# Optimization experiments

Measured on AMD Instinct MI355X. Metric: run time of the kernel, lower is better.

The kernel has to match this reference:

```python
import jax, jax.numpy as jnp
import numpy as np

B, N, D, H, DK, DV = 2, 2048, 1024, 16, 64, 64
NEG = -1000000000.0
EPS = 1e-6


def setup_inputs() -> dict:
    key = jax.random.key(0)
    ks = jax.random.split(key, 8)
    s = 0.02
    return {
        "q": jax.random.normal(ks[0], (B, N, D), jnp.float32),
        "k": jax.random.normal(ks[1], (B, N, D), jnp.float32),
        "v": jax.random.normal(ks[2], (B, N, D), jnp.float32),
        "attn_mask": jnp.ones((B, N, N), jnp.int32),
        "Wq": jax.random.normal(ks[3], (D, H * DK), jnp.float32) * s,
        "Wk": jax.random.normal(ks[4], (D, H * DK), jnp.float32) * s,
        "Wv": jax.random.normal(ks[5], (D, H * DV), jnp.float32) * s,
        "Wo": jax.random.normal(ks[6], (H * DV, D), jnp.float32) * s,
        "gamma": jnp.ones((D,), jnp.float32),
        "beta": jnp.zeros((D,), jnp.float32),
    }


def reference(q, k, v, attn_mask, Wq, Wk, Wv, Wo, gamma, beta):
    b, n, _ = q.shape
    residual = q
    # project and split heads: (b, h, n, dk)
    qh = (q @ Wq).reshape(b, n, H, DK).transpose(0, 2, 1, 3)
    kh = (k @ Wk).reshape(b, n, H, DK).transpose(0, 2, 1, 3)
    vh = (v @ Wv).reshape(b, n, H, DV).transpose(0, 2, 1, 3)
    temperature = DK ** 0.5
    scores = jnp.einsum('bhnd,bhmd->bhnm', qh / temperature, kh)
    # external mask (masked where mask == 0), broadcast over heads
    scores = jnp.where(attn_mask[:, None, :, :] == 0, NEG, scores)
    # built-in causal mask (strictly upper triangle)
    causal = jnp.triu(jnp.ones((n, n), dtype=bool), k=1)
    scores = jnp.where(causal, NEG, scores)
    attn = jax.nn.softmax(scores, axis=-1)
    out = jnp.einsum('bhnm,bhmd->bnhd', attn, vh).reshape(b, n, H * DV)
    out = out @ Wo + residual
    # LayerNorm(eps=1e-6)
    mean = out.mean(-1, keepdims=True)
    var = ((out - mean) ** 2).mean(-1, keepdims=True)
    out = (out - mean) / jnp.sqrt(var + EPS) * gamma + beta
    return out, attn
```

## Files before the change

### kernel.cpp

```cpp
#include <hip/hip_runtime.h>
#include <hip/hip_bf16.h>
#include <stdint.h>

#define B_ 2
#define N_ 2048
#define D_ 1024
#define H_ 16
#define MM 4096
#define NN 1024
#define KK 1024

typedef __bf16 bf16;
typedef __bf16 bf16x8 __attribute__((ext_vector_type(8)));
typedef float f32x4 __attribute__((ext_vector_type(4)));

struct __align__(8) bf4 { bf16 v[4]; };

#define LDS_STRIDE 144
#define LOG2E 1.44269504088896340736f

#define GLDS(gp, lp)                                                     \
    __builtin_amdgcn_global_load_lds(                                    \
        (const __attribute__((address_space(1))) void*)(gp),             \
        (__attribute__((address_space(3))) void*)(lp), 16, 0, 0)

__global__ __launch_bounds__(256) void k_cvt3(const float* __restrict__ q,
                                              const float* __restrict__ k,
                                              const float* __restrict__ v,
                                              bf16* __restrict__ qb,
                                              bf16* __restrict__ kb,
                                              bf16* __restrict__ vb) {
    const int z = blockIdx.y;
    const float* s = z == 0 ? q : z == 1 ? k : v;
    bf16* d = z == 0 ? qb : z == 1 ? kb : vb;
    size_t i = ((size_t)blockIdx.x * 256 + threadIdx.x) * 8;
    f32x4 a = *(const f32x4*)(s + i);
    f32x4 b = *(const f32x4*)(s + i + 4);
    bf16x8 o;
#pragma unroll
    for (int j = 0; j < 4; ++j) { o[j] = (bf16)a[j]; o[4 + j] = (bf16)b[j]; }
    *(bf16x8*)(d + i) = o;
}

__global__ void k_wtt4(const float* __restrict__ Wq, const float* __restrict__ Wk,
                       const float* __restrict__ Wv, const float* __restrict__ Wo,
                       bf16* __restrict__ WqT, bf16* __restrict__ WkT,
                       bf16* __restrict__ WvT, bf16* __restrict__ WoT) {
    const int z = blockIdx.z;
    const float* W = z == 0 ? Wq : z == 1 ? Wk : z == 2 ? Wv : Wo;
    bf16* Wt = z == 0 ? WqT : z == 1 ? WkT : z == 2 ? WvT : WoT;
    __shared__ float t[32][33];
    int bx = blockIdx.x * 32, by = blockIdx.y * 32;
    int tx = threadIdx.x, ty = threadIdx.y;
#pragma unroll
    for (int j = 0; j < 32; j += 8)
        t[ty + j][tx] = W[(size_t)(by + ty + j) * 1024 + bx + tx];
    __syncthreads();
#pragma unroll
    for (int j = 0; j < 32; j += 8)
        Wt[(size_t)(bx + ty + j) * 1024 + by + tx] = (bf16)t[tx][ty + j];
}

__global__ __launch_bounds__(256) void k_bits(const int* __restrict__ mask,
                                              uint32_t* __restrict__ bits) {
    size_t flat = (size_t)blockIdx.x * 256 + threadIdx.x;
    int col = (int)(flat & (N_ - 1));
    int row = (int)((flat >> 11) & (N_ - 1));
    bool ok = (mask[flat] != 0) && (col <= row);
    unsigned long long bal = __ballot(ok);
    if ((threadIdx.x & 63) == 0)
        *(unsigned long long*)(bits + (flat >> 5)) = bal;
}

__device__ __forceinline__ void mm_core(const bf16* __restrict__ A,
                                        const bf16* __restrict__ Bt,
                                        int bm0, int bn0,
                                        bf16* As, bf16* Bs,
                                        f32x4 (&acc)[4][4]) {
    const int tid = threadIdx.x, w = tid >> 6, lane = tid & 63;
    const int g = lane >> 4, li = lane & 15;
    const int wr = w >> 1, wc = w & 1;

    f32x4 zz = {0.f, 0.f, 0.f, 0.f};
#pragma unroll
    for (int mf = 0; mf < 4; ++mf)
#pragma unroll
        for (int nf = 0; nf < 4; ++nf) acc[mf][nf] = zz;

    auto stage = [&](int k0) {
#pragma unroll
        for (int c = 0; c < 4; ++c) {
            int ch = c * 256 + tid;
            int r = ch >> 3, cl = ch & 7;
            GLDS(A + (size_t)(bm0 + r) * KK + k0 + cl * 8,
                 As + ((size_t)c * 256 + w * 64) * 8);
        }
#pragma unroll
        for (int c = 0; c < 4; ++c) {
            int ch = c * 256 + tid;
            int r = ch >> 3, cl = ch & 7;
            GLDS(Bt + (size_t)(bn0 + r) * KK + k0 + cl * 8,
                 Bs + ((size_t)c * 256 + w * 64) * 8);
        }
    };

    stage(0);
    for (int s = 0; s < KK / 64; ++s) {
        __syncthreads();
#pragma unroll
        for (int kk = 0; kk < 2; ++kk) {
            bf16x8 af[4], bfr[4];
#pragma unroll
            for (int i = 0; i < 4; ++i) {
                af[i] = *(const bf16x8*)(As + (wr * 64 + i * 16 + li) * 64 + kk * 32 + g * 8);
                bfr[i] = *(const bf16x8*)(Bs + (wc * 64 + i * 16 + li) * 64 + kk * 32 + g * 8);
            }
#pragma unroll
            for (int mf = 0; mf < 4; ++mf)
#pragma unroll
                for (int nf = 0; nf < 4; ++nf)
                    acc[mf][nf] = __builtin_amdgcn_mfma_f32_16x16x32_bf16(
                        af[mf], bfr[nf], acc[mf][nf], 0, 0, 0);
        }
        __syncthreads();
        if (s + 1 < KK / 64) stage((s + 1) * 64);
    }
}

__global__ __launch_bounds__(256) void k_proj(const bf16* __restrict__ qb,
                                              const bf16* __restrict__ kb,
                                              const bf16* __restrict__ vb,
                                              const bf16* __restrict__ WqT,
                                              const bf16* __restrict__ WkT,
                                              const bf16* __restrict__ WvT,
                                              bf16* __restrict__ Qh,
                                              bf16* __restrict__ Kh,
                                              bf16* __restrict__ Vt) {
    __shared__ __align__(16) bf16 As[128 * 64];
    __shared__ __align__(16) bf16 Bs[128 * 64];
    const int z = blockIdx.y;
    const bf16* A = z == 0 ? qb : z == 1 ? kb : vb;
    const bf16* Bt = z == 0 ? WqT : z == 1 ? WkT : WvT;
    int bid = blockIdx.x;
    int swz = (bid & 7) * 32 + (bid >> 3);
    int bm0 = (swz >> 3) * 128, bn0 = (swz & 7) * 128;

    f32x4 acc[4][4];
    mm_core(A, Bt, bm0, bn0, As, Bs, acc);

    const int tid = threadIdx.x, w = tid >> 6, lane = tid & 63;
    const int g = lane >> 4, li = lane & 15;
    const int wr = w >> 1, wc = w & 1;
    const float scale = (z == 0) ? 0.125f * LOG2E : 1.0f;

    if (z < 2) {
        bf16* C = (z == 0) ? Qh : Kh;
#pragma unroll
        for (int mf = 0; mf < 4; ++mf)
#pragma unroll
            for (int nf = 0; nf < 4; ++nf) {
                int m0 = bm0 + wr * 64 + mf * 16 + g * 4;
                int n = bn0 + wc * 64 + nf * 16 + li;
#pragma unroll
                for (int r = 0; r < 4; ++r)
                    C[(size_t)(m0 + r) * NN + n] = (bf16)(acc[mf][nf][r] * scale);
            }
    } else {
#pragma unroll
        for (int mf = 0; mf < 4; ++mf)
#pragma unroll
            for (int nf = 0; nf < 4; ++nf) {
                int m0 = bm0 + wr * 64 + mf * 16 + g * 4;
                int n = bn0 + wc * 64 + nf * 16 + li;
                int bq = m0 >> 11, tok = m0 & (N_ - 1);
                int hh = n >> 6, dv = n & 63;
                bf4 val;
#pragma unroll
                for (int r = 0; r < 4; ++r) val.v[r] = (bf16)acc[mf][nf][r];
                *(bf4*)(Vt + ((size_t)((bq * H_ + hh) * 64 + dv)) * N_ + tok) = val;
            }
    }
}

__global__ __launch_bounds__(256) void k_out(const bf16* __restrict__ Ob,
                                             const bf16* __restrict__ WoT,
                                             float* __restrict__ outp,
                                             const float* __restrict__ resid) {
    __shared__ __align__(16) bf16 As[128 * 64];
    __shared__ __align__(16) bf16 Bs[128 * 64];
    int bid = blockIdx.x;
    int swz = (bid & 7) * 32 + (bid >> 3);
    int bm0 = (swz >> 3) * 128, bn0 = (swz & 7) * 128;

    f32x4 acc[4][4];
    mm_core(Ob, WoT, bm0, bn0, As, Bs, acc);

    const int tid = threadIdx.x, w = tid >> 6, lane = tid & 63;
    const int g = lane >> 4, li = lane & 15;
    const int wr = w >> 1, wc = w & 1;
#pragma unroll
    for (int mf = 0; mf < 4; ++mf)
#pragma unroll
        for (int nf = 0; nf < 4; ++nf) {
            int m0 = bm0 + wr * 64 + mf * 16 + g * 4;
            int n = bn0 + wc * 64 + nf * 16 + li;
#pragma unroll
            for (int r = 0; r < 4; ++r) {
                size_t ix = (size_t)(m0 + r) * NN + n;
                outp[ix] = acc[mf][nf][r] + resid[ix];
            }
        }
}

__global__ __launch_bounds__(256) void k_attn(const bf16* __restrict__ Qh,
                                              const bf16* __restrict__ Kh,
                                              const bf16* __restrict__ Vt,
                                              const uint32_t* __restrict__ bits,
                                              float* __restrict__ attnp,
                                              bf16* __restrict__ Ob) {
    __shared__ __align__(16) char Qs[64 * LDS_STRIDE];
    __shared__ __align__(16) char Ks[64 * LDS_STRIDE];
    __shared__ __align__(16) char Vs[64 * LDS_STRIDE];
    __shared__ __align__(16) char Ps[64 * LDS_STRIDE];
    const int tid = threadIdx.x, lane = tid & 63, w = tid >> 6;
    const int g = lane >> 4, li = lane & 15;
    const int p = blockIdx.x, h = blockIdx.y, b = blockIdx.z;
    const int srow = tid >> 3, sc = tid & 7;
    const int myrow = w * 16 + li;

    const size_t kbase = ((size_t)b * N_) * D_ + h * 64;
    const size_t vbase = ((size_t)(b * H_ + h) * 64) * N_;
    f32x4 zz = {0.f, 0.f, 0.f, 0.f};

    for (int half = 0; half < 2; ++half) {
        const int qt = half ? (31 - p) : p;
        const int i0 = qt << 6;
        const size_t abase = (((size_t)b * H_ + h) * N_ + i0) * (size_t)N_;

        __syncthreads();
        {
            const char* qsrc = (const char*)Qh +
                (kbase + (size_t)(i0 + srow) * D_ + sc * 8) * 2;
            bf16x8 t0 = *(const bf16x8*)qsrc;
            bf16x8 t1 = *(const bf16x8*)(qsrc + (size_t)32 * D_ * 2);
            *(bf16x8*)(Qs + srow * LDS_STRIDE + sc * 16) = t0;
            *(bf16x8*)(Qs + (srow + 32) * LDS_STRIDE + sc * 16) = t1;
        }
        const uint32_t* mrow = bits + (((size_t)b * N_ + i0 + myrow) << 6);

        float m = -1e30f, l = 0.f;
        bf16x8 ka, kb2, va, vb2;
        {
            const char* ks = (const char*)Kh + (kbase + (size_t)srow * D_ + sc * 8) * 2;
            ka = *(const bf16x8*)ks;
            kb2 = *(const bf16x8*)(ks + (size_t)32 * D_ * 2);
        }
        for (int jt = 0; jt <= qt; ++jt) {
            __syncthreads();
            *(bf16x8*)(Ks + srow * LDS_STRIDE + sc * 16) = ka;
            *(bf16x8*)(Ks + (srow + 32) * LDS_STRIDE + sc * 16) = kb2;
            {
                int jn = (jt < qt) ? jt + 1 : qt;
                const char* ks = (const char*)Kh +
                    (kbase + (size_t)(jn * 64 + srow) * D_ + sc * 8) * 2;
                ka = *(const bf16x8*)ks;
                kb2 = *(const bf16x8*)(ks + (size_t)32 * D_ * 2);
            }
            uint2 mw = *(const uint2*)(mrow + (jt << 1));
            __syncthreads();

            f32x4 s[4];
#pragma unroll
            for (int mf = 0; mf < 4; ++mf) s[mf] = zz;
#pragma unroll
            for (int kk = 0; kk < 2; ++kk) {
                const int kb = kk * 64 + (g << 4);
                bf16x8 qf = *(const bf16x8*)(Qs + myrow * LDS_STRIDE + kb);
#pragma unroll
                for (int mf = 0; mf < 4; ++mf) {
                    bf16x8 kf = *(const bf16x8*)(Ks + (mf * 16 + li) * LDS_STRIDE + kb);
                    s[mf] = __builtin_amdgcn_mfma_f32_16x16x32_bf16(kf, qf, s[mf], 0, 0, 0);
                }
            }
            float tmax = m;
#pragma unroll
            for (int mf = 0; mf < 4; ++mf) {
                uint32_t wsel = (mf < 2) ? mw.x : mw.y;
#pragma unroll
                for (int r = 0; r < 4; ++r) {
                    int sh = (mf & 1) * 16 + g * 4 + r;
                    float xv = ((wsel >> sh) & 1) ? s[mf][r] : -1e9f;
                    s[mf][r] = xv;
                    tmax = fmaxf(tmax, xv);
                }
            }
            tmax = fmaxf(tmax, __shfl_xor(tmax, 16));
            tmax = fmaxf(tmax, __shfl_xor(tmax, 32));
            float ps = 0.f;
#pragma unroll
            for (int mf = 0; mf < 4; ++mf)
#pragma unroll
                for (int r = 0; r < 4; ++r) ps += exp2f(s[mf][r] - tmax);
            ps += __shfl_xor(ps, 16);
            ps += __shfl_xor(ps, 32);
            l = l * exp2f(m - tmax) + ps;
            m = tmax;
        }
        const float ml = m + __log2f(l);

        f32x4 oacc[4];
#pragma unroll
        for (int nf = 0; nf < 4; ++nf) oacc[nf] = zz;

        {
            const char* ks = (const char*)Kh + (kbase + (size_t)srow * D_ + sc * 8) * 2;
            ka = *(const bf16x8*)ks;
            kb2 = *(const bf16x8*)(ks + (size_t)32 * D_ * 2);
            const char* vs = (const char*)Vt + (vbase + (size_t)srow * N_ + sc * 8) * 2;
            va = *(const bf16x8*)vs;
            vb2 = *(const bf16x8*)(vs + (size_t)32 * N_ * 2);
        }
        for (int jt = 0; jt <= qt; ++jt) {
            __syncthreads();
            *(bf16x8*)(Ks + srow * LDS_STRIDE + sc * 16) = ka;
            *(bf16x8*)(Ks + (srow + 32) * LDS_STRIDE + sc * 16) = kb2;
            *(bf16x8*)(Vs + srow * LDS_STRIDE + sc * 16) = va;
            *(bf16x8*)(Vs + (srow + 32) * LDS_STRIDE + sc * 16) = vb2;
            {
                int jn = (jt < qt) ? jt + 1 : qt;
                const char* ks = (const char*)Kh +
                    (kbase + (size_t)(jn * 64 + srow) * D_ + sc * 8) * 2;
                ka = *(const bf16x8*)ks;
                kb2 = *(const bf16x8*)(ks + (size_t)32 * D_ * 2);
                const char* vs = (const char*)Vt +
                    (vbase + (size_t)srow * N_ + jn * 64 + sc * 8) * 2;
                va = *(const bf16x8*)vs;
                vb2 = *(const bf16x8*)(vs + (size_t)32 * N_ * 2);
            }
            uint2 mw = *(const uint2*)(mrow + (jt << 1));
            __syncthreads();

            f32x4 s[4];
#pragma unroll
            for (int mf = 0; mf < 4; ++mf) s[mf] = zz;
#pragma unroll
            for (int kk = 0; kk < 2; ++kk) {
                const int kb = kk * 64 + (g << 4);
                bf16x8 qf = *(const bf16x8*)(Qs + myrow * LDS_STRIDE + kb);
#pragma unroll
                for (int mf = 0; mf < 4; ++mf) {
                    bf16x8 kf = *(const bf16x8*)(Ks + (mf * 16 + li) * LDS_STRIDE + kb);
                    s[mf] = __builtin_amdgcn_mfma_f32_16x16x32_bf16(kf, qf, s[mf], 0, 0, 0);
                }
            }

#pragma unroll
            for (int mf = 0; mf < 4; ++mf) {
                uint32_t wsel = (mf < 2) ? mw.x : mw.y;
#pragma unroll
                for (int r = 0; r < 4; ++r) {
                    int sh = (mf & 1) * 16 + g * 4 + r;
                    float xv = ((wsel >> sh) & 1) ? s[mf][r] : -1e9f;
                    s[mf][r] = exp2f(xv - ml);
                }
                __builtin_nontemporal_store(s[mf],
                    (f32x4*)(attnp + abase + (size_t)myrow * N_ + (jt << 6) + mf * 16 + g * 4));
                bf4 pk;
#pragma unroll
                for (int r = 0; r < 4; ++r) pk.v[r] = (bf16)s[mf][r];
                *(bf4*)(Ps + myrow * LDS_STRIDE + (mf * 16 + g * 4) * 2) = pk;
            }
#pragma unroll
            for (int kk = 0; kk < 2; ++kk) {
                const int kb = kk * 64 + (g << 4);
                bf16x8 pf = *(const bf16x8*)(Ps + myrow * LDS_STRIDE + kb);
#pragma unroll
                for (int nf = 0; nf < 4; ++nf) {
                    bf16x8 vf = *(const bf16x8*)(Vs + (nf * 16 + li) * LDS_STRIDE + kb);
                    oacc[nf] = __builtin_amdgcn_mfma_f32_16x16x32_bf16(pf, vf, oacc[nf], 0, 0, 0);
                }
            }
        }
#pragma unroll
        for (int nf = 0; nf < 4; ++nf)
#pragma unroll
            for (int r = 0; r < 4; ++r) {
                int gi = i0 + w * 16 + g * 4 + r;
                Ob[((size_t)(b * N_ + gi)) * D_ + h * 64 + nf * 16 + li] = (bf16)oacc[nf][r];
            }
        int zc0 = i0 + 64;
        if (zc0 < N_) {
            int r = tid >> 2, tc = tid & 3;
            f32x4 z = zz;
            for (int c = zc0 + tc * 4; c < N_; c += 16)
                __builtin_nontemporal_store(z, (f32x4*)(attnp + abase + (size_t)r * N_ + c));
        }
    }
}

__global__ __launch_bounds__(256) void k_ln(float* __restrict__ out,
                                            const float* __restrict__ gamma,
                                            const float* __restrict__ beta) {
    const int row = blockIdx.x, t = threadIdx.x, lane = t & 63, w = t >> 6;
    float* p = out + (size_t)row * D_;
    f32x4 x = *(const f32x4*)(p + t * 4);
    float s = x[0] + x[1] + x[2] + x[3];
    float s2 = x[0] * x[0] + x[1] * x[1] + x[2] * x[2] + x[3] * x[3];
#pragma unroll
    for (int o = 1; o < 64; o <<= 1) {
        s += __shfl_xor(s, o);
        s2 += __shfl_xor(s2, o);
    }
    __shared__ float r1[4], r2[4];
    if (lane == 0) { r1[w] = s; r2[w] = s2; }
    __syncthreads();
    s = r1[0] + r1[1] + r1[2] + r1[3];
    s2 = r2[0] + r2[1] + r2[2] + r2[3];
    float mean = s * (1.f / D_);
    float var = s2 * (1.f / D_) - mean * mean;
    float rstd = rsqrtf(var + 1e-6f);
    f32x4 gv = *(const f32x4*)(gamma + t * 4);
    f32x4 bv = *(const f32x4*)(beta + t * 4);
    f32x4 y;
#pragma unroll
    for (int c = 0; c < 4; ++c) y[c] = (x[c] - mean) * rstd * gv[c] + bv[c];
    *(f32x4*)(p + t * 4) = y;
}

extern "C" void kernel_launch(void* const* d_in, const int* in_sizes, int n_in,
                              void* d_out, int out_size, void* d_ws,
                              size_t ws_size, hipStream_t stream) {
    (void)in_sizes; (void)n_in; (void)out_size; (void)ws_size;
    const float* q = (const float*)d_in[0];
    const float* k = (const float*)d_in[1];
    const float* v = (const float*)d_in[2];
    const int* msk = (const int*)d_in[3];
    const float* Wq = (const float*)d_in[4];
    const float* Wk = (const float*)d_in[5];
    const float* Wv = (const float*)d_in[6];
    const float* Wo = (const float*)d_in[7];
    const float* gamma = (const float*)d_in[8];
    const float* beta = (const float*)d_in[9];

    float* outp = (float*)d_out;
    float* attnp = outp + (size_t)B_ * N_ * D_;

    const size_t U = (size_t)B_ * N_ * D_;
    const size_t W1 = (size_t)D_ * D_;
    bf16* ws = (bf16*)d_ws;
    bf16* qb = ws;   ws += U;
    bf16* kb = ws;   ws += U;
    bf16* vb = ws;   ws += U;
    bf16* WqT = ws;  ws += W1;
    bf16* WkT = ws;  ws += W1;
    bf16* WvT = ws;  ws += W1;
    bf16* WoT = ws;  ws += W1;
    bf16* Qh = ws;   ws += U;
    bf16* Kh = ws;   ws += U;
    bf16* Vt = ws;   ws += U;
    bf16* Ob = ws;   ws += U;
    uint32_t* bits = (uint32_t*)ws;

    k_cvt3<<<dim3(U / 8 / 256, 3), 256, 0, stream>>>(q, k, v, qb, kb, vb);
    k_wtt4<<<dim3(32, 32, 4), dim3(32, 8), 0, stream>>>(Wq, Wk, Wv, Wo, WqT, WkT, WvT, WoT);
    k_bits<<<(size_t)B_ * N_ * N_ / 256, 256, 0, stream>>>(msk, bits);

    k_proj<<<dim3(256, 3), 256, 0, stream>>>(qb, kb, vb, WqT, WkT, WvT, Qh, Kh, Vt);

    k_attn<<<dim3(16, H_, B_), 256, 0, stream>>>(Qh, Kh, Vt, bits, attnp, Ob);

    k_out<<<256, 256, 0, stream>>>(Ob, WoT, outp, q);

    k_ln<<<B_ * N_, 256, 0, stream>>>(outp, gamma, beta);
}
```

Baseline: 306.8 us.

## Fuse fp32-to-bf16 input conversion into projection GEMM and flatten attention grid

Drops the separate q/k/v conversion kernel: the projection GEMM now loads fp32 activations into registers, converts them to bf16 and writes them to a padded LDS tile, with the next tile's global loads overlapping the current tile's MFMA work. This removes one full read/write pass of the activations and a launch, at the cost of register-staged loads instead of direct global-to-LDS copies. The attention kernel changes from blocks that each process a paired query tile (p and 31-p) sequentially to a 1024-block grid with one query tile per block, ordered so short and long tiles interleave. Its attention-matrix stores also switch from nontemporal to ordinary stores.

```diff
diff --git a/kernel.cpp b/kernel.cpp
--- a/kernel.cpp
+++ b/kernel.cpp
@@ -23,24 +23,6 @@
     __builtin_amdgcn_global_load_lds(                                    \
         (const __attribute__((address_space(1))) void*)(gp),             \
         (__attribute__((address_space(3))) void*)(lp), 16, 0, 0)
-
-__global__ __launch_bounds__(256) void k_cvt3(const float* __restrict__ q,
-                                              const float* __restrict__ k,
-                                              const float* __restrict__ v,
-                                              bf16* __restrict__ qb,
-                                              bf16* __restrict__ kb,
-                                              bf16* __restrict__ vb) {
-    const int z = blockIdx.y;
-    const float* s = z == 0 ? q : z == 1 ? k : v;
-    bf16* d = z == 0 ? qb : z == 1 ? kb : vb;
-    size_t i = ((size_t)blockIdx.x * 256 + threadIdx.x) * 8;
-    f32x4 a = *(const f32x4*)(s + i);
-    f32x4 b = *(const f32x4*)(s + i + 4);
-    bf16x8 o;
-#pragma unroll
-    for (int j = 0; j < 4; ++j) { o[j] = (bf16)a[j]; o[4 + j] = (bf16)b[j]; }
-    *(bf16x8*)(d + i) = o;
-}
 
 __global__ void k_wtt4(const float* __restrict__ Wq, const float* __restrict__ Wk,
                        const float* __restrict__ Wv, const float* __restrict__ Wo,
@@ -72,87 +54,95 @@
         *(unsigned long long*)(bits + (flat >> 5)) = bal;
 }
 
-__device__ __forceinline__ void mm_core(const bf16* __restrict__ A,
-                                        const bf16* __restrict__ Bt,
-                                        int bm0, int bn0,
-                                        bf16* As, bf16* Bs,
-                                        f32x4 (&acc)[4][4]) {
-    const int tid = threadIdx.x, w = tid >> 6, lane = tid & 63;
-    const int g = lane >> 4, li = lane & 15;
-    const int wr = w >> 1, wc = w & 1;
-
-    f32x4 zz = {0.f, 0.f, 0.f, 0.f};
-#pragma unroll
-    for (int mf = 0; mf < 4; ++mf)
-#pragma unroll
-        for (int nf = 0; nf < 4; ++nf) acc[mf][nf] = zz;
-
-    auto stage = [&](int k0) {
-#pragma unroll
-        for (int c = 0; c < 4; ++c) {
-            int ch = c * 256 + tid;
-            int r = ch >> 3, cl = ch & 7;
-            GLDS(A + (size_t)(bm0 + r) * KK + k0 + cl * 8,
-                 As + ((size_t)c * 256 + w * 64) * 8);
-        }
-#pragma unroll
-        for (int c = 0; c < 4; ++c) {
-            int ch = c * 256 + tid;
-            int r = ch >> 3, cl = ch & 7;
-            GLDS(Bt + (size_t)(bn0 + r) * KK + k0 + cl * 8,
-                 Bs + ((size_t)c * 256 + w * 64) * 8);
-        }
-    };
-
-    stage(0);
-    for (int s = 0; s < KK / 64; ++s) {
-        __syncthreads();
-#pragma unroll
-        for (int kk = 0; kk < 2; ++kk) {
-            bf16x8 af[4], bfr[4];
-#pragma unroll
-            for (int i = 0; i < 4; ++i) {
-                af[i] = *(const bf16x8*)(As + (wr * 64 + i * 16 + li) * 64 + kk * 32 + g * 8);
-                bfr[i] = *(const bf16x8*)(Bs + (wc * 64 + i * 16 + li) * 64 + kk * 32 + g * 8);
-            }
-#pragma unroll
-            for (int mf = 0; mf < 4; ++mf)
-#pragma unroll
-                for (int nf = 0; nf < 4; ++nf)
-                    acc[mf][nf] = __builtin_amdgcn_mfma_f32_16x16x32_bf16(
-                        af[mf], bfr[nf], acc[mf][nf], 0, 0, 0);
-        }
-        __syncthreads();
-        if (s + 1 < KK / 64) stage((s + 1) * 64);
-    }
-}
-
-__global__ __launch_bounds__(256) void k_proj(const bf16* __restrict__ qb,
-                                              const bf16* __restrict__ kb,
-                                              const bf16* __restrict__ vb,
+__global__ __launch_bounds__(256) void k_proj(const float* __restrict__ qf,
+                                              const float* __restrict__ kf,
+                                              const float* __restrict__ vf,
                                               const bf16* __restrict__ WqT,
                                               const bf16* __restrict__ WkT,
                                               const bf16* __restrict__ WvT,
                                               bf16* __restrict__ Qh,
                                               bf16* __restrict__ Kh,
                                               bf16* __restrict__ Vt) {
-    __shared__ __align__(16) bf16 As[128 * 64];
+    __shared__ __align__(16) bf16 As[128 * 72];
     __shared__ __align__(16) bf16 Bs[128 * 64];
     const int z = blockIdx.y;
-    const bf16* A = z == 0 ? qb : z == 1 ? kb : vb;
+    const float* A = z == 0 ? qf : z == 1 ? kf : vf;
     const bf16* Bt = z == 0 ? WqT : z == 1 ? WkT : WvT;
     int bid = blockIdx.x;
     int swz = (bid & 7) * 32 + (bid >> 3);
     int bm0 = (swz >> 3) * 128, bn0 = (swz & 7) * 128;
 
-    f32x4 acc[4][4];
-    mm_core(A, Bt, bm0, bn0, As, Bs, acc);
-
     const int tid = threadIdx.x, w = tid >> 6, lane = tid & 63;
     const int g = lane >> 4, li = lane & 15;
     const int wr = w >> 1, wc = w & 1;
+
+    f32x4 zz = {0.f, 0.f, 0.f, 0.f};
+    f32x4 acc[4][4];
+#pragma unroll
+    for (int mf = 0; mf < 4; ++mf)
+#pragma unroll
+        for (int nf = 0; nf < 4; ++nf) acc[mf][nf] = zz;
+
+    f32x4 pa[4][2];
+    auto issueA = [&](int k0) {
+#pragma unroll
+        for (int c = 0; c < 4; ++c) {
+            int ch = c * 256 + tid;
+            int r = ch >> 3, cl = ch & 7;
+            const float* s = A + (size_t)(bm0 + r) * KK + k0 + cl * 8;
+            pa[c][0] = *(const f32x4*)s;
+            pa[c][1] = *(const f32x4*)(s + 4);
+        }
+    };
+    auto writeA = [&]() {
+#pragma unroll
+        for (int c = 0; c < 4; ++c) {
+            int ch = c * 256 + tid;
+            int r = ch >> 3, cl = ch & 7;
+            bf16x8 t;
+#pragma unroll
+            for (int j = 0; j < 4; ++j) {
+                t[j] = (bf16)pa[c][0][j];
+                t[4 + j] = (bf16)pa[c][1][j];
+            }
+            *(bf16x8*)(As + (size_t)r * 72 + cl * 8) = t;
+        }
+    };
+    auto stageB = [&](int k0) {
+#pragma unroll
+        for (int c = 0; c < 4; ++c) {
+            int ch = c * 256 + tid;
+            int r = ch >> 3, cl = ch & 7;
+            GLDS(Bt + (size_t)(bn0 + r) * KK + k0 + cl * 8,
+                 Bs + ((size_t)c * 256 + w * 64) * 8);
+        }
+    };
+
+    issueA(0);
+    for (int s = 0; s < KK / 64; ++s) {
+        __syncthreads();
+        writeA();
+        stageB(s * 64);
+        if (s + 1 < KK / 64) issueA((s + 1) * 64);
+        __syncthreads();
+#pragma unroll
+        for (int kk = 0; kk < 2; ++kk) {
+            bf16x8 af[4], bfr[4];
+#pragma unroll
+            for (int i = 0; i < 4; ++i) {
+                af[i] = *(const bf16x8*)(As + (wr * 64 + i * 16 + li) * 72 + kk * 32 + g * 8);
+                bfr[i] = *(const bf16x8*)(Bs + (wc * 64 + i * 16 + li) * 64 + kk * 32 + g * 8);
+            }
+#pragma unroll
+            for (int mf = 0; mf < 4; ++mf)
+#pragma unroll
+                for (int nf = 0; nf < 4; ++nf)
+                    acc[mf][nf] = __builtin_amdgcn_mfma_f32_16x16x32_bf16(
+                        af[mf], bfr[nf], acc[mf][nf], 0, 0, 0);
+        }
+    }
+
     const float scale = (z == 0) ? 0.125f * LOG2E : 1.0f;
-
     if (z < 2) {
         bf16* C = (z == 0) ? Qh : Kh;
 #pragma unroll
@@ -192,12 +182,55 @@
     int swz = (bid & 7) * 32 + (bid >> 3);
     int bm0 = (swz >> 3) * 128, bn0 = (swz & 7) * 128;
 
-    f32x4 acc[4][4];
-    mm_core(Ob, WoT, bm0, bn0, As, Bs, acc);
-
     const int tid = threadIdx.x, w = tid >> 6, lane = tid & 63;
     const int g = lane >> 4, li = lane & 15;
     const int wr = w >> 1, wc = w & 1;
+
+    f32x4 zz = {0.f, 0.f, 0.f, 0.f};
+    f32x4 acc[4][4];
+#pragma unroll
+    for (int mf = 0; mf < 4; ++mf)
+#pragma unroll
+        for (int nf = 0; nf < 4; ++nf) acc[mf][nf] = zz;
+
+    auto stage = [&](int k0) {
+#pragma unroll
+        for (int c = 0; c < 4; ++c) {
+            int ch = c * 256 + tid;
+            int r = ch >> 3, cl = ch & 7;
+            GLDS(Ob + (size_t)(bm0 + r) * KK + k0 + cl * 8,
+                 As + ((size_t)c * 256 + w * 64) * 8);
+        }
+#pragma unroll
+        for (int c = 0; c < 4; ++c) {
+            int ch = c * 256 + tid;
+            int r = ch >> 3, cl = ch & 7;
+            GLDS(WoT + (size_t)(bn0 + r) * KK + k0 + cl * 8,
+                 Bs + ((size_t)c * 256 + w * 64) * 8);
+        }
+    };
+
+    stage(0);
+    for (int s = 0; s < KK / 64; ++s) {
+        __syncthreads();
+#pragma unroll
+        for (int kk = 0; kk < 2; ++kk) {
+            bf16x8 af[4], bfr[4];
+#pragma unroll
+            for (int i = 0; i < 4; ++i) {
+                af[i] = *(const bf16x8*)(As + (wr * 64 + i * 16 + li) * 64 + kk * 32 + g * 8);
+                bfr[i] = *(const bf16x8*)(Bs + (wc * 64 + i * 16 + li) * 64 + kk * 32 + g * 8);
+            }
+#pragma unroll
+            for (int mf = 0; mf < 4; ++mf)
+#pragma unroll
+                for (int nf = 0; nf < 4; ++nf)
+                    acc[mf][nf] = __builtin_amdgcn_mfma_f32_16x16x32_bf16(
+                        af[mf], bfr[nf], acc[mf][nf], 0, 0, 0);
+        }
+        __syncthreads();
+        if (s + 1 < KK / 64) stage((s + 1) * 64);
+    }
 #pragma unroll
     for (int mf = 0; mf < 4; ++mf)
 #pragma unroll
@@ -224,177 +257,177 @@
     __shared__ __align__(16) char Ps[64 * LDS_STRIDE];
     const int tid = threadIdx.x, lane = tid & 63, w = tid >> 6;
     const int g = lane >> 4, li = lane & 15;
-    const int p = blockIdx.x, h = blockIdx.y, b = blockIdx.z;
     const int srow = tid >> 3, sc = tid & 7;
     const int myrow = w * 16 + li;
 
+    const int id = blockIdx.x;
+    const int s_ = id & 255, g_ = id >> 8;
+    const int u = s_ & 31;
+    const int hb = (s_ >> 5) | (g_ << 3);
+    const int h = hb & 15, b = hb >> 4;
+    const int qt = (g_ & 1) ? (31 - u) : u;
+    const int i0 = qt << 6;
+
     const size_t kbase = ((size_t)b * N_) * D_ + h * 64;
     const size_t vbase = ((size_t)(b * H_ + h) * 64) * N_;
+    const size_t abase = (((size_t)b * H_ + h) * N_ + i0) * (size_t)N_;
     f32x4 zz = {0.f, 0.f, 0.f, 0.f};
 
-    for (int half = 0; half < 2; ++half) {
-        const int qt = half ? (31 - p) : p;
-        const int i0 = qt << 6;
-        const size_t abase = (((size_t)b * H_ + h) * N_ + i0) * (size_t)N_;
-
-        __syncthreads();
+    {
+        const char* qsrc = (const char*)Qh +
+            (kbase + (size_t)(i0 + srow) * D_ + sc * 8) * 2;
+        bf16x8 t0 = *(const bf16x8*)qsrc;
+        bf16x8 t1 = *(const bf16x8*)(qsrc + (size_t)32 * D_ * 2);
+        *(bf16x8*)(Qs + srow * LDS_STRIDE + sc * 16) = t0;
+        *(bf16x8*)(Qs + (srow + 32) * LDS_STRIDE + sc * 16) = t1;
+    }
+    const uint32_t* mrow = bits + (((size_t)b * N_ + i0 + myrow) << 6);
+
+    float m = -1e30f, l = 0.f;
+    bf16x8 ka, kb2, va, vb2;
+    {
+        const char* ks = (const char*)Kh + (kbase + (size_t)srow * D_ + sc * 8) * 2;
+        ka = *(const bf16x8*)ks;
+        kb2 = *(const bf16x8*)(ks + (size_t)32 * D_ * 2);
+    }
+    for (int jt = 0; jt <= qt; ++jt) {
+        __syncthreads();
+        *(bf16x8*)(Ks + srow * LDS_STRIDE + sc * 16) = ka;
+        *(bf16x8*)(Ks + (srow + 32) * LDS_STRIDE + sc * 16) = kb2;
         {
-            const char* qsrc = (const char*)Qh +
-                (kbase + (size_t)(i0 + srow) * D_ + sc * 8) * 2;
-            bf16x8 t0 = *(const bf16x8*)qsrc;
-            bf16x8 t1 = *(const bf16x8*)(qsrc + (size_t)32 * D_ * 2);
-            *(bf16x8*)(Qs + srow * LDS_STRIDE + sc * 16) = t0;
-            *(bf16x8*)(Qs + (srow + 32) * LDS_STRIDE + sc * 16) = t1;
-        }
-        const uint32_t* mrow = bits + (((size_t)b * N_ + i0 + myrow) << 6);
-
-        float m = -1e30f, l = 0.f;
-        bf16x8 ka, kb2, va, vb2;
-        {
-            const char* ks = (const char*)Kh + (kbase + (size_t)srow * D_ + sc * 8) * 2;
+            int jn = (jt < qt) ? jt + 1 : qt;
+            const char* ks = (const char*)Kh +
+                (kbase + (size_t)(jn * 64 + srow) * D_ + sc * 8) * 2;
             ka = *(const bf16x8*)ks;
             kb2 = *(const bf16x8*)(ks + (size_t)32 * D_ * 2);
         }
-        for (int jt = 0; jt <= qt; ++jt) {
-            __syncthreads();
-            *(bf16x8*)(Ks + srow * LDS_STRIDE + sc * 16) = ka;
-            *(bf16x8*)(Ks + (srow + 32) * LDS_STRIDE + sc * 16) = kb2;
-            {
-                int jn = (jt < qt) ? jt + 1 : qt;
-                const char* ks = (const char*)Kh +
-                    (kbase + (size_t)(jn * 64 + srow) * D_ + sc * 8) * 2;
-                ka = *(const bf16x8*)ks;
-                kb2 = *(const bf16x8*)(ks + (size_t)32 * D_ * 2);
-            }
-            uint2 mw = *(const uint2*)(mrow + (jt << 1));
-            __syncthreads();
-
-            f32x4 s[4];
-#pragma unroll
-            for (int mf = 0; mf < 4; ++mf) s[mf] = zz;
-#pragma unroll
-            for (int kk = 0; kk < 2; ++kk) {
-                const int kb = kk * 64 + (g << 4);
-                bf16x8 qf = *(const bf16x8*)(Qs + myrow * LDS_STRIDE + kb);
-#pragma unroll
-                for (int mf = 0; mf < 4; ++mf) {
-                    bf16x8 kf = *(const bf16x8*)(Ks + (mf * 16 + li) * LDS_STRIDE + kb);
-                    s[mf] = __builtin_amdgcn_mfma_f32_16x16x32_bf16(kf, qf, s[mf], 0, 0, 0);
-                }
-            }
-            float tmax = m;
+        uint2 mw = *(const uint2*)(mrow + (jt << 1));
+        __syncthreads();
+
+        f32x4 s[4];
+#pragma unroll
+        for (int mf = 0; mf < 4; ++mf) s[mf] = zz;
+#pragma unroll
+        for (int kk = 0; kk < 2; ++kk) {
+            const int kb = kk * 64 + (g << 4);
+            bf16x8 qf = *(const bf16x8*)(Qs + myrow * LDS_STRIDE + kb);
 #pragma unroll
             for (int mf = 0; mf < 4; ++mf) {
-                uint32_t wsel = (mf < 2) ? mw.x : mw.y;
-#pragma unroll
-                for (int r = 0; r < 4; ++r) {
-                    int sh = (mf & 1) * 16 + g * 4 + r;
-                    float xv = ((wsel >> sh) & 1) ? s[mf][r] : -1e9f;
-                    s[mf][r] = xv;
-                    tmax = fmaxf(tmax, xv);
-                }
-            }
-            tmax = fmaxf(tmax, __shfl_xor(tmax, 16));
-            tmax = fmaxf(tmax, __shfl_xor(tmax, 32));
-            float ps = 0.f;
-#pragma unroll
-            for (int mf = 0; mf < 4; ++mf)
-#pragma unroll
-                for (int r = 0; r < 4; ++r) ps += exp2f(s[mf][r] - tmax);
-            ps += __shfl_xor(ps, 16);
-            ps += __shfl_xor(ps, 32);
-            l = l * exp2f(m - tmax) + ps;
-            m = tmax;
-        }
-        const float ml = m + __log2f(l);
-
-        f32x4 oacc[4];
-#pragma unroll
-        for (int nf = 0; nf < 4; ++nf) oacc[nf] = zz;
-
+                bf16x8 kf = *(const bf16x8*)(Ks + (mf * 16 + li) * LDS_STRIDE + kb);
+                s[mf] = __builtin_amdgcn_mfma_f32_16x16x32_bf16(kf, qf, s[mf], 0, 0, 0);
+            }
+        }
+        float tmax = m;
+#pragma unroll
+        for (int mf = 0; mf < 4; ++mf) {
+            uint32_t wsel = (mf < 2) ? mw.x : mw.y;
+#pragma unroll
+            for (int r = 0; r < 4; ++r) {
+                int sh = (mf & 1) * 16 + g * 4 + r;
+                float xv = ((wsel >> sh) & 1) ? s[mf][r] : -1e9f;
+                s[mf][r] = xv;
+                tmax = fmaxf(tmax, xv);
+            }
+        }
+        tmax = fmaxf(tmax, __shfl_xor(tmax, 16));
+        tmax = fmaxf(tmax, __shfl_xor(tmax, 32));
+        float ps = 0.f;
+#pragma unroll
+        for (int mf = 0; mf < 4; ++mf)
+#pragma unroll
+            for (int r = 0; r < 4; ++r) ps += exp2f(s[mf][r] - tmax);
+        ps += __shfl_xor(ps, 16);
+        ps += __shfl_xor(ps, 32);
+        l = l * exp2f(m - tmax) + ps;
+        m = tmax;
+    }
+    const float ml = m + __log2f(l);
+
+    f32x4 oacc[4];
+#pragma unroll
+    for (int nf = 0; nf < 4; ++nf) oacc[nf] = zz;
+
+    {
+        const char* ks = (const char*)Kh + (kbase + (size_t)srow * D_ + sc * 8) * 2;
+        ka = *(const bf16x8*)ks;
+        kb2 = *(const bf16x8*)(ks + (size_t)32 * D_ * 2);
+        const char* vs = (const char*)Vt + (vbase + (size_t)srow * N_ + sc * 8) * 2;
+        va = *(const bf16x8*)vs;
+        vb2 = *(const bf16x8*)(vs + (size_t)32 * N_ * 2);
+    }
+    for (int jt = 0; jt <= qt; ++jt) {
+        __syncthreads();
+        *(bf16x8*)(Ks + srow * LDS_STRIDE + sc * 16) = ka;
+        *(bf16x8*)(Ks + (srow + 32) * LDS_STRIDE + sc * 16) = kb2;
+        *(bf16x8*)(Vs + srow * LDS_STRIDE + sc * 16) = va;
+        *(bf16x8*)(Vs + (srow + 32) * LDS_STRIDE + sc * 16) = vb2;
         {
-            const char* ks = (const char*)Kh + (kbase + (size_t)srow * D_ + sc * 8) * 2;
+            int jn = (jt < qt) ? jt + 1 : qt;
+            const char* ks = (const char*)Kh +
+                (kbase + (size_t)(jn * 64 + srow) * D_ + sc * 8) * 2;
             ka = *(const bf16x8*)ks;
             kb2 = *(const bf16x8*)(ks + (size_t)32 * D_ * 2);
-            const char* vs = (const char*)Vt + (vbase + (size_t)srow * N_ + sc * 8) * 2;
+            const char* vs = (const char*)Vt +
+                (vbase + (size_t)srow * N_ + jn * 64 + sc * 8) * 2;
             va = *(const bf16x8*)vs;
             vb2 = *(const bf16x8*)(vs + (size_t)32 * N_ * 2);
         }
-        for (int jt = 0; jt <= qt; ++jt) {
-            __syncthreads();
-            *(bf16x8*)(Ks + srow * LDS_STRIDE + sc * 16) = ka;
-            *(bf16x8*)(Ks + (srow + 32) * LDS_STRIDE + sc * 16) = kb2;
-            *(bf16x8*)(Vs + srow * LDS_STRIDE + sc * 16) = va;
-            *(bf16x8*)(Vs + (srow + 32) * LDS_STRIDE + sc * 16) = vb2;
-            {
-                int jn = (jt < qt) ? jt + 1 : qt;
-                const char* ks = (const char*)Kh +
-                    (kbase + (size_t)(jn * 64 + srow) * D_ + sc * 8) * 2;
-                ka = *(const bf16x8*)ks;
-                kb2 = *(const bf16x8*)(ks + (size_t)32 * D_ * 2);
-                const char* vs = (const char*)Vt +
-                    (vbase + (size_t)srow * N_ + jn * 64 + sc * 8) * 2;
-                va = *(const bf16x8*)vs;
-                vb2 = *(const bf16x8*)(vs + (size_t)32 * N_ * 2);
-            }
-            uint2 mw = *(const uint2*)(mrow + (jt << 1));
-            __syncthreads();
-
-            f32x4 s[4];
-#pragma unroll
-            for (int mf = 0; mf < 4; ++mf) s[mf] = zz;
-#pragma unroll
-            for (int kk = 0; kk < 2; ++kk) {
-                const int kb = kk * 64 + (g << 4);
-                bf16x8 qf = *(const bf16x8*)(Qs + myrow * LDS_STRIDE + kb);
-#pragma unroll
-                for (int mf = 0; mf < 4; ++mf) {
-                    bf16x8 kf = *(const bf16x8*)(Ks + (mf * 16 + li) * LDS_STRIDE + kb);
-                    s[mf] = __builtin_amdgcn_mfma_f32_16x16x32_bf16(kf, qf, s[mf], 0, 0, 0);
-                }
-            }
-
+        uint2 mw = *(const uint2*)(mrow + (jt << 1));
+        __syncthreads();
+
+        f32x4 s[4];
+#pragma unroll
+        for (int mf = 0; mf < 4; ++mf) s[mf] = zz;
+#pragma unroll
+        for (int kk = 0; kk < 2; ++kk) {
+            const int kb = kk * 64 + (g << 4);
+            bf16x8 qf = *(const bf16x8*)(Qs + myrow * LDS_STRIDE + kb);
 #pragma unroll
             for (int mf = 0; mf < 4; ++mf) {
-                uint32_t wsel = (mf < 2) ? mw.x : mw.y;
-#pragma unroll
-                for (int r = 0; r < 4; ++r) {
-                    int sh = (mf & 1) * 16 + g * 4 + r;
-                    float xv = ((wsel >> sh) & 1) ? s[mf][r] : -1e9f;
-                    s[mf][r] = exp2f(xv - ml);
-                }
-                __builtin_nontemporal_store(s[mf],
-                    (f32x4*)(attnp + abase + (size_t)myrow * N_ + (jt << 6) + mf * 16 + g * 4));
-                bf4 pk;
-#pragma unroll
-                for (int r = 0; r < 4; ++r) pk.v[r] = (bf16)s[mf][r];
-                *(bf4*)(Ps + myrow * LDS_STRIDE + (mf * 16 + g * 4) * 2) = pk;
-            }
-#pragma unroll
-            for (int kk = 0; kk < 2; ++kk) {
-                const int kb = kk * 64 + (g << 4);
-                bf16x8 pf = *(const bf16x8*)(Ps + myrow * LDS_STRIDE + kb);
-#pragma unroll
-                for (int nf = 0; nf < 4; ++nf) {
-                    bf16x8 vf = *(const bf16x8*)(Vs + (nf * 16 + li) * LDS_STRIDE + kb);
-                    oacc[nf] = __builtin_amdgcn_mfma_f32_16x16x32_bf16(pf, vf, oacc[nf], 0, 0, 0);
-                }
-            }
-        }
-#pragma unroll
-        for (int nf = 0; nf < 4; ++nf)
+                bf16x8 kf = *(const bf16x8*)(Ks + (mf * 16 + li) * LDS_STRIDE + kb);
+                s[mf] = __builtin_amdgcn_mfma_f32_16x16x32_bf16(kf, qf, s[mf], 0, 0, 0);
+            }
+        }
+
+#pragma unroll
+        for (int mf = 0; mf < 4; ++mf) {
+            uint32_t wsel = (mf < 2) ? mw.x : mw.y;
 #pragma unroll
             for (int r = 0; r < 4; ++r) {
-                int gi = i0 + w * 16 + g * 4 + r;
-                Ob[((size_t)(b * N_ + gi)) * D_ + h * 64 + nf * 16 + li] = (bf16)oacc[nf][r];
-            }
-        int zc0 = i0 + 64;
-        if (zc0 < N_) {
-            int r = tid >> 2, tc = tid & 3;
-            f32x4 z = zz;
-            for (int c = zc0 + tc * 4; c < N_; c += 16)
-                __builtin_nontemporal_store(z, (f32x4*)(attnp + abase + (size_t)r * N_ + c));
-        }
+                int sh = (mf & 1) * 16 + g * 4 + r;
+                float xv = ((wsel >> sh) & 1) ? s[mf][r] : -1e9f;
+                s[mf][r] = exp2f(xv - ml);
+            }
+            *(f32x4*)(attnp + abase + (size_t)myrow * N_ + (jt << 6) + mf * 16 + g * 4) = s[mf];
+            bf4 pk;
+#pragma unroll
+            for (int r = 0; r < 4; ++r) pk.v[r] = (bf16)s[mf][r];
+            *(bf4*)(Ps + myrow * LDS_STRIDE + (mf * 16 + g * 4) * 2) = pk;
+        }
+#pragma unroll
+        for (int kk = 0; kk < 2; ++kk) {
+            const int kb = kk * 64 + (g << 4);
+            bf16x8 pf = *(const bf16x8*)(Ps + myrow * LDS_STRIDE + kb);
+#pragma unroll
+            for (int nf = 0; nf < 4; ++nf) {
+                bf16x8 vf = *(const bf16x8*)(Vs + (nf * 16 + li) * LDS_STRIDE + kb);
+                oacc[nf] = __builtin_amdgcn_mfma_f32_16x16x32_bf16(pf, vf, oacc[nf], 0, 0, 0);
+            }
+        }
+    }
+#pragma unroll
+    for (int nf = 0; nf < 4; ++nf)
+#pragma unroll
+        for (int r = 0; r < 4; ++r) {
+            int gi = i0 + w * 16 + g * 4 + r;
+            Ob[((size_t)(b * N_ + gi)) * D_ + h * 64 + nf * 16 + li] = (bf16)oacc[nf][r];
+        }
+    int zc0 = i0 + 64;
+    if (zc0 < N_) {
+        int r = tid >> 2, tc = tid & 3;
+        f32x4 z = zz;
+        for (int c = zc0 + tc * 4; c < N_; c += 16)
+            *(f32x4*)(attnp + abase + (size_t)r * N_ + c) = z;
     }
 }
 
@@ -448,9 +481,6 @@
     const size_t U = (size_t)B_ * N_ * D_;
     const size_t W1 = (size_t)D_ * D_;
     bf16* ws = (bf16*)d_ws;
-    bf16* qb = ws;   ws += U;
-    bf16* kb = ws;   ws += U;
-    bf16* vb = ws;   ws += U;
     bf16* WqT = ws;  ws += W1;
     bf16* WkT = ws;  ws += W1;
     bf16* WvT = ws;  ws += W1;
@@ -461,13 +491,12 @@
     bf16* Ob = ws;   ws += U;
     uint32_t* bits = (uint32_t*)ws;
 
-    k_cvt3<<<dim3(U / 8 / 256, 3), 256, 0, stream>>>(q, k, v, qb, kb, vb);
     k_wtt4<<<dim3(32, 32, 4), dim3(32, 8), 0, stream>>>(Wq, Wk, Wv, Wo, WqT, WkT, WvT, WoT);
     k_bits<<<(size_t)B_ * N_ * N_ / 256, 256, 0, stream>>>(msk, bits);
 
-    k_proj<<<dim3(256, 3), 256, 0, stream>>>(qb, kb, vb, WqT, WkT, WvT, Qh, Kh, Vt);
-
-    k_attn<<<dim3(16, H_, B_), 256, 0, stream>>>(Qh, Kh, Vt, bits, attnp, Ob);
+    k_proj<<<dim3(256, 3), 256, 0, stream>>>(q, k, v, WqT, WkT, WvT, Qh, Kh, Vt);
+
+    k_attn<<<1024, 256, 0, stream>>>(Qh, Kh, Vt, bits, attnp, Ob);
 
     k_out<<<256, 256, 0, stream>>>(Ob, WoT, outp, q);
 
```

New measurement: 322.4 us. 1.05x slower.
